# Optimization experiments

Hardware: AMD Instinct MI355X
Metric: run time of the kernel (lower is better)

## Reference

```python
import jax, jax.numpy as jnp
import numpy as np

HEADS = 4
DIM_HEAD = 32
DIM = 128
HIDDEN = HEADS * DIM_HEAD  # 128
SCALE = 10
EPS = 1e-12  # matches F.normalize default eps


def l2_norm(t):
    # normalize along last axis (heads axis after the port's reshape)
    n = jnp.sqrt(jnp.sum(t * t, axis=-1, keepdims=True))
    return t / jnp.maximum(n, EPS)


def setup_inputs() -> dict:
    key = jax.random.key(0)
    k1, k2, k3 = jax.random.split(key, 3)
    b, h, w = 4, 16, 256
    x = jax.random.normal(k1, (b, h, w, DIM), dtype=jnp.float32)
    # 1x1 conv kernels collapse to dense matrices on the channel axis
    w_qkv = jax.random.normal(k2, (DIM, 3 * HIDDEN), dtype=jnp.float32) / np.sqrt(DIM).astype(np.float32)
    w_out = jax.random.normal(k3, (HIDDEN, DIM), dtype=jnp.float32) / np.sqrt(HIDDEN).astype(np.float32)
    b_out = jnp.zeros((DIM,), dtype=jnp.float32)
    return {"x": x, "w_qkv": w_qkv, "w_out": w_out, "b_out": b_out}


def reference(x, w_qkv, w_out, b_out):
    b, h, w, c = x.shape
    n = h * w
    # 1x1 conv (no bias) -> qkv, split on channel axis
    qkv = jnp.einsum('bhwc,cf->bhwf', x, w_qkv)
    q, k, v = jnp.split(qkv, 3, axis=-1)
    # faithful port reshape: (b, h, w, hidden) -> (b, dim_head, n, heads)
    q = q.reshape(b, -1, n, HEADS)
    k = k.reshape(b, -1, n, HEADS)
    v = v.reshape(b, -1, n, HEADS)
    q = l2_norm(q)  # computed but unused downstream, as in the source
    k = l2_norm(k)
    # sim: contract over dim_head axis -> (b, n, n, heads)
    sim = jnp.einsum('bhdn,bhen->bden', k, v) * SCALE
    attn = jax.nn.softmax(sim, axis=-2)
    # out: contract attn with v over spatial axis -> (b, n, dim_head, heads)
    out = jnp.einsum('bedh,bndh->benh', attn, v)
    out = out.reshape(b, h, w, HIDDEN)
    # final 1x1 conv with bias
    return jnp.einsum('bhwf,fo->bhwo', out, w_out) + b_out
```

## Files before the change

kernel.cpp:

```cpp
#include <hip/hip_runtime.h>
#include <math.h>


#define SEQ 4096
#define PAIR_ELEMS (SEQ * 32)

typedef __attribute__((ext_vector_type(8))) short bf16x8;
typedef __attribute__((ext_vector_type(4))) float f32x4;

static __device__ __forceinline__ unsigned short f2bf(float x) {
    unsigned u = __float_as_uint(x);
    u += 0x7fffu + ((u >> 16) & 1u);
    return (unsigned short)(u >> 16);
}
static __device__ __forceinline__ float bf2f(unsigned short h) {
    return __uint_as_float(((unsigned)h) << 16);
}

__global__ __launch_bounds__(256) void kv_kernel(const float* __restrict__ x,
                                                 const float* __restrict__ wqkv,
                                                 unsigned short* __restrict__ Qhi,
                                                 unsigned short* __restrict__ Qlo,
                                                 unsigned short* __restrict__ Mhi,
                                                 unsigned short* __restrict__ Mlo,
                                                 unsigned short* __restrict__ Mpv2) {
    __shared__ __align__(16) float xs[32][128];
    __shared__ __align__(8) unsigned short vstage[32][128];

    const int b    = blockIdx.x >> 7;
    const int p7   = blockIdx.x & 127;
    const int t    = threadIdx.x;
    const int half = t >> 7;
    const int u    = t & 127;
    const int q    = u & 31;
    const int rg   = u >> 5;
    const int woff = 128 + (half << 7) + (q << 2);

    {
        const float* xb = x + ((size_t)(b * SEQ + p7)) * 128;
#pragma unroll
        for (int uu = 0; uu < 4; ++uu) {
            int idx = t + (uu << 8);
            int j   = idx >> 5;
            int c4  = idx & 31;
            *(float4*)&xs[j][c4 * 4] =
                *(const float4*)(xb + (size_t)j * (128 * 128) + c4 * 4);
        }
    }
    __syncthreads();

    float acc[8][4];
#pragma unroll
    for (int jr = 0; jr < 8; ++jr)
#pragma unroll
        for (int a = 0; a < 4; ++a) acc[jr][a] = 0.f;

    float4 wA[4], wB[4];
#pragma unroll
    for (int i = 0; i < 4; ++i)
        wA[i] = *(const float4*)(wqkv + (size_t)i * 384 + woff);

    auto gstep = [&](float4 (&wcur)[4], float4 (&wnxt)[4], int i4) {
        const int i4n = (i4 + 4) & 127;
#pragma unroll
        for (int i = 0; i < 4; ++i)
            wnxt[i] = *(const float4*)(wqkv + (size_t)(i4n + i) * 384 + woff);
#pragma unroll
        for (int jr = 0; jr < 8; ++jr) {
            float4 xv = *(const float4*)&xs[8 * rg + jr][i4];
            acc[jr][0] = fmaf(xv.x, wcur[0].x, acc[jr][0]);
            acc[jr][1] = fmaf(xv.x, wcur[0].y, acc[jr][1]);
            acc[jr][2] = fmaf(xv.x, wcur[0].z, acc[jr][2]);
            acc[jr][3] = fmaf(xv.x, wcur[0].w, acc[jr][3]);
            acc[jr][0] = fmaf(xv.y, wcur[1].x, acc[jr][0]);
            acc[jr][1] = fmaf(xv.y, wcur[1].y, acc[jr][1]);
            acc[jr][2] = fmaf(xv.y, wcur[1].z, acc[jr][2]);
            acc[jr][3] = fmaf(xv.y, wcur[1].w, acc[jr][3]);
            acc[jr][0] = fmaf(xv.z, wcur[2].x, acc[jr][0]);
            acc[jr][1] = fmaf(xv.z, wcur[2].y, acc[jr][1]);
            acc[jr][2] = fmaf(xv.z, wcur[2].z, acc[jr][2]);
            acc[jr][3] = fmaf(xv.z, wcur[2].w, acc[jr][3]);
            acc[jr][0] = fmaf(xv.w, wcur[3].x, acc[jr][0]);
            acc[jr][1] = fmaf(xv.w, wcur[3].y, acc[jr][1]);
            acc[jr][2] = fmaf(xv.w, wcur[3].z, acc[jr][2]);
            acc[jr][3] = fmaf(xv.w, wcur[3].w, acc[jr][3]);
        }
    };
    for (int i4 = 0; i4 < 128; i4 += 8) {
        gstep(wA, wB, i4);
        gstep(wB, wA, i4 + 4);
    }

    const int pairbase = b << 2;
    const int de = (p7 << 5) + q;

    if (half == 0) {
        float qn[8][4];
#pragma unroll
        for (int jr = 0; jr < 8; ++jr) {
            float s = acc[jr][0] * acc[jr][0] + acc[jr][1] * acc[jr][1]
                    + acc[jr][2] * acc[jr][2] + acc[jr][3] * acc[jr][3];
            float inv = 14.426950408889634f / fmaxf(sqrtf(s), 1e-12f);
#pragma unroll
            for (int a = 0; a < 4; ++a) qn[jr][a] = acc[jr][a] * inv;
        }
#pragma unroll
        for (int a = 0; a < 4; ++a) {
            unsigned hi[4], lo[4];
#pragma unroll
            for (int j2 = 0; j2 < 4; ++j2) {
                float v0 = qn[2 * j2][a], v1 = qn[2 * j2 + 1][a];
                unsigned short h0 = f2bf(v0), h1 = f2bf(v1);
                hi[j2] = (unsigned)h0 | ((unsigned)h1 << 16);
                lo[j2] = (unsigned)f2bf(v0 - bf2f(h0))
                       | ((unsigned)f2bf(v1 - bf2f(h1)) << 16);
            }
            size_t off = (size_t)(pairbase + a) * PAIR_ELEMS + (size_t)de * 32 + 8 * rg;
            *(uint4*)(Qhi + off) = make_uint4(hi[0], hi[1], hi[2], hi[3]);
            *(uint4*)(Qlo + off) = make_uint4(lo[0], lo[1], lo[2], lo[3]);
        }
    } else {
#pragma unroll
        for (int a = 0; a < 4; ++a) {
            unsigned hi[4], lo[4];
#pragma unroll
            for (int j2 = 0; j2 < 4; ++j2) {
                float v0 = acc[2 * j2][a], v1 = acc[2 * j2 + 1][a];
                unsigned short h0 = f2bf(v0), h1 = f2bf(v1);
                hi[j2] = (unsigned)h0 | ((unsigned)h1 << 16);
                lo[j2] = (unsigned)f2bf(v0 - bf2f(h0))
                       | ((unsigned)f2bf(v1 - bf2f(h1)) << 16);
            }
            size_t off = (size_t)(pairbase + a) * PAIR_ELEMS + (size_t)de * 32 + 8 * rg;
            *(uint4*)(Mhi + off) = make_uint4(hi[0], hi[1], hi[2], hi[3]);
            *(uint4*)(Mlo + off) = make_uint4(lo[0], lo[1], lo[2], lo[3]);
        }
#pragma unroll
        for (int jr = 0; jr < 8; ++jr) {
            unsigned short h0 = f2bf(acc[jr][0]);
            unsigned short h1 = f2bf(acc[jr][1]);
            unsigned short h2 = f2bf(acc[jr][2]);
            unsigned short h3 = f2bf(acc[jr][3]);
            *(uint2*)&vstage[8 * rg + jr][4 * q] =
                make_uint2((unsigned)h0 | ((unsigned)h1 << 16),
                           (unsigned)h2 | ((unsigned)h3 << 16));
        }
    }
    __syncthreads();

    unsigned* mpv32 = (unsigned*)Mpv2;
#pragma unroll
    for (int uu = 0; uu < 8; ++uu) {
        int task = t + (uu << 8);
        int w  = task & 15;
        int jj = (task >> 4) & 31;
        int aa = task >> 9;
        unsigned lo = vstage[jj][(w << 3) + aa];
        unsigned hi = vstage[jj][(w << 3) + 4 + aa];
        int pr = (b << 2) + aa;
        size_t dst = (size_t)pr * 65536 + (size_t)jj * 2048
                   + ((size_t)(p7 >> 1)) * 32
                   + (size_t)((p7 & 1) * 16)
                   + (size_t)(((w >> 1) & 3) * 4)
                   + (size_t)((w >> 3) * 2)
                   + (size_t)(w & 1);
        mpv32[dst] = lo | (hi << 16);
    }
}

__global__ __launch_bounds__(256, 2) void attn_kernel(const unsigned short* __restrict__ Qhi,
                                                      const unsigned short* __restrict__ Qlo,
                                                      const unsigned short* __restrict__ Mhi,
                                                      const unsigned short* __restrict__ Mlo,
                                                      const unsigned short* __restrict__ Mpv2,
                                                      unsigned short* __restrict__ outb) {
    const int bid  = blockIdx.x;
    const int pair = ((bid & 7) << 1) + (bid >> 8);
    const int dblk = (bid & 255) >> 3;
    const int t    = threadIdx.x;
    const int wid  = t >> 6;
    const int lane = t & 63;
    const int col  = lane & 15;
    const int g    = lane >> 4;
    const int d0   = dblk * 128 + wid * 32;

    const size_t pb = (size_t)pair * PAIR_ELEMS;

    bf16x8 ah[2], al[2];
#pragma unroll
    for (int s = 0; s < 2; ++s) {
        size_t o = pb + (size_t)(d0 + 16 * s + col) * 32 + g * 8;
        ah[s] = *(const bf16x8*)(Qhi + o);
        al[s] = *(const bf16x8*)(Qlo + o);
    }

    const unsigned short* mh = Mhi + pb;
    const unsigned short* ml = Mlo + pb;
    const unsigned short* mp = Mpv2 + pb;
    const f32x4 z = {0.f, 0.f, 0.f, 0.f};

    float rmax[2] = {-3e38f, -3e38f};
    {
        bf16x8 pA[4], pB[4];
#pragma unroll
        for (int cc = 0; cc < 4; ++cc)
            pA[cc] = *(const bf16x8*)(mh + (size_t)(16 * cc + col) * 32 + g * 8);

        auto sweep = [&](bf16x8 (&cur)[4], bf16x8 (&nxt)[4], int e0) {
            const int en = (e0 + 64) & (SEQ - 1);
#pragma unroll
            for (int cc = 0; cc < 4; ++cc)
                nxt[cc] = *(const bf16x8*)(mh + (size_t)(en + 16 * cc + col) * 32 + g * 8);
#pragma unroll
            for (int cc = 0; cc < 4; ++cc) {
#pragma unroll
                for (int s = 0; s < 2; ++s) {
                    f32x4 sv = __builtin_amdgcn_mfma_f32_16x16x32_bf16(cur[cc], ah[s], z, 0, 0, 0);
                    rmax[s] = fmaxf(rmax[s], fmaxf(fmaxf(sv[0], sv[1]), fmaxf(sv[2], sv[3])));
                }
            }
        };
        for (int e0 = 0; e0 < SEQ; e0 += 128) {
            sweep(pA, pB, e0);
            sweep(pB, pA, e0 + 64);
        }
    }
#pragma unroll
    for (int s = 0; s < 2; ++s) {
        float m = rmax[s];
        m = fmaxf(m, __shfl_xor(m, 16));
        m = fmaxf(m, __shfl_xor(m, 32));
        rmax[s] = m;
    }
    f32x4 minit[2];
#pragma unroll
    for (int s = 0; s < 2; ++s)
        minit[s] = (f32x4){-rmax[s], -rmax[s], -rmax[s], -rmax[s]};

    f32x4 O[2][2];
    float lsum[2] = {0.f, 0.f};
#pragma unroll
    for (int s = 0; s < 2; ++s)
#pragma unroll
        for (int nh = 0; nh < 2; ++nh) O[s][nh] = (f32x4){0.f, 0.f, 0.f, 0.f};

    {
        bf16x8 tA[12], tB[12];
#pragma unroll
        for (int cc = 0; cc < 4; ++cc) {
            size_t ro = (size_t)(16 * cc + col) * 32 + g * 8;
            tA[cc]     = *(const bf16x8*)(mh + ro);
            tA[4 + cc] = *(const bf16x8*)(ml + ro);
        }
#pragma unroll
        for (int nh = 0; nh < 2; ++nh)
#pragma unroll
            for (int m = 0; m < 2; ++m)
                tA[8 + 2 * nh + m] =
                    *(const bf16x8*)(mp + (size_t)(16 * nh + col) * SEQ + 32 * m + 8 * g);

        auto flash = [&](bf16x8 (&cur)[12], bf16x8 (&nxt)[12], int e0) {
            const int en = (e0 + 64) & (SEQ - 1);
#pragma unroll
            for (int cc = 0; cc < 4; ++cc) {
                size_t ro = (size_t)(en + 16 * cc + col) * 32 + g * 8;
                nxt[cc]     = *(const bf16x8*)(mh + ro);
                nxt[4 + cc] = *(const bf16x8*)(ml + ro);
            }
#pragma unroll
            for (int nh = 0; nh < 2; ++nh)
#pragma unroll
                for (int m = 0; m < 2; ++m)
                    nxt[8 + 2 * nh + m] =
                        *(const bf16x8*)(mp + (size_t)(16 * nh + col) * SEQ
                                         + en + 32 * m + 8 * g);

            f32x4 S[2][4];
#pragma unroll
            for (int cc = 0; cc < 4; ++cc) {
#pragma unroll
                for (int s = 0; s < 2; ++s) {
                    f32x4 tac = __builtin_amdgcn_mfma_f32_16x16x32_bf16(cur[4 + cc], ah[s], minit[s], 0, 0, 0);
                    tac = __builtin_amdgcn_mfma_f32_16x16x32_bf16(cur[cc], al[s], tac, 0, 0, 0);
                    S[s][cc] = __builtin_amdgcn_mfma_f32_16x16x32_bf16(cur[cc], ah[s], tac, 0, 0, 0);
                }
            }
            unsigned pw[2][4][2];
#pragma unroll
            for (int s = 0; s < 2; ++s) {
#pragma unroll
                for (int cc = 0; cc < 4; ++cc) {
                    float p0 = __builtin_amdgcn_exp2f(S[s][cc][0]);
                    float p1 = __builtin_amdgcn_exp2f(S[s][cc][1]);
                    float p2 = __builtin_amdgcn_exp2f(S[s][cc][2]);
                    float p3 = __builtin_amdgcn_exp2f(S[s][cc][3]);
                    lsum[s] += (p0 + p1) + (p2 + p3);
                    asm("v_cvt_pk_bf16_f32 %0, %1, %2" : "=v"(pw[s][cc][0]) : "v"(p0), "v"(p1));
                    asm("v_cvt_pk_bf16_f32 %0, %1, %2" : "=v"(pw[s][cc][1]) : "v"(p2), "v"(p3));
                }
            }
#pragma unroll
            for (int s = 0; s < 2; ++s) {
#pragma unroll
                for (int m = 0; m < 2; ++m) {
                    unsigned pk4[4] = {pw[s][2 * m][0], pw[s][2 * m][1],
                                       pw[s][2 * m + 1][0], pw[s][2 * m + 1][1]};
                    bf16x8 pbf = *(bf16x8*)pk4;
                    O[s][0] = __builtin_amdgcn_mfma_f32_16x16x32_bf16(cur[8 + 0 + m], pbf, O[s][0], 0, 0, 0);
                    O[s][1] = __builtin_amdgcn_mfma_f32_16x16x32_bf16(cur[8 + 2 + m], pbf, O[s][1], 0, 0, 0);
                }
            }
        };
        for (int e0 = 0; e0 < SEQ; e0 += 128) {
            flash(tA, tB, e0);
            flash(tB, tA, e0 + 64);
        }
    }

#pragma unroll
    for (int s = 0; s < 2; ++s) {
        float l = lsum[s];
        l += __shfl_xor(l, 16);
        l += __shfl_xor(l, 32);
        lsum[s] = l;
    }

    const int bb = pair >> 2;
    const int aa = pair & 3;
#pragma unroll
    for (int s = 0; s < 2; ++s) {
        float inv = 1.0f / lsum[s];
        size_t rowb = ((size_t)(bb * SEQ + d0 + 16 * s + col)) * 128;
#pragma unroll
        for (int nh = 0; nh < 2; ++nh) {
#pragma unroll
            for (int r = 0; r < 4; ++r) {
                int n = 16 * nh + 4 * g + r;
                outb[rowb + n * 4 + aa] = f2bf(O[s][nh][r] * inv);
            }
        }
    }
}

__global__ __launch_bounds__(256) void out_kernel(const unsigned short* __restrict__ opre,
                                                  const float* __restrict__ wout,
                                                  const float* __restrict__ bout,
                                                  float* __restrict__ y) {
    __shared__ __align__(16) float xs[8][128];
    const int r0 = blockIdx.x * 8;
    const int t  = threadIdx.x;
    {
        const unsigned* src = (const unsigned*)(opre + (size_t)r0 * 128);
        unsigned v0 = src[t * 2], v1 = src[t * 2 + 1];
        float* dst = &xs[0][0] + t * 4;
        dst[0] = bf2f((unsigned short)(v0 & 0xffff));
        dst[1] = bf2f((unsigned short)(v0 >> 16));
        dst[2] = bf2f((unsigned short)(v1 & 0xffff));
        dst[3] = bf2f((unsigned short)(v1 >> 16));
    }
    __syncthreads();

    const int c  = t & 127;
    const int rh = (t >> 7) * 4;
    float acc[4] = {0.f, 0.f, 0.f, 0.f};

    for (int i = 0; i < 128; i += 4) {
        float w0 = wout[(i + 0) * 128 + c];
        float w1 = wout[(i + 1) * 128 + c];
        float w2 = wout[(i + 2) * 128 + c];
        float w3 = wout[(i + 3) * 128 + c];
#pragma unroll
        for (int p = 0; p < 4; ++p) {
            float4 xp = *(const float4*)&xs[rh + p][i];
            acc[p] = fmaf(xp.x, w0, acc[p]);
            acc[p] = fmaf(xp.y, w1, acc[p]);
            acc[p] = fmaf(xp.z, w2, acc[p]);
            acc[p] = fmaf(xp.w, w3, acc[p]);
        }
    }
    float bb = bout[c];
#pragma unroll
    for (int p = 0; p < 4; ++p) {
        y[((size_t)(r0 + rh + p)) * 128 + c] = acc[p] + bb;
    }
}

extern "C" void kernel_launch(void* const* d_in, const int* in_sizes, int n_in,
                              void* d_out, int out_size, void* d_ws, size_t ws_size,
                              hipStream_t stream) {
    const float* x    = (const float*)d_in[0];
    const float* wqkv = (const float*)d_in[1];
    const float* wout = (const float*)d_in[2];
    const float* bout = (const float*)d_in[3];
    float* y = (float*)d_out;

    unsigned short* Qhi = (unsigned short*)d_ws;
    unsigned short* Qlo = Qhi + (size_t)16 * PAIR_ELEMS;
    unsigned short* Mhi = Qlo + (size_t)16 * PAIR_ELEMS;
    unsigned short* Mlo = Mhi + (size_t)16 * PAIR_ELEMS;
    unsigned short* Mpv2 = Mlo + (size_t)16 * PAIR_ELEMS;
    unsigned short* outb = Mpv2 + (size_t)16 * PAIR_ELEMS;

    kv_kernel<<<512, 256, 0, stream>>>(x, wqkv, Qhi, Qlo, Mhi, Mlo, Mpv2);
    attn_kernel<<<512, 256, 0, stream>>>(Qhi, Qlo, Mhi, Mlo, Mpv2, outb);
    out_kernel<<<2048, 256, 0, stream>>>(outb, wout, bout, y);
}
```

Baseline: 270.3 us.

## Split attention over key halves with merge kernel and double kv_kernel grid

The attention kernel can now split the sequence dimension into two halves (split-K flash style), writing partial outputs plus max/sum statistics that a new merge kernel combines. This doubles the grid from 512 to 1024 blocks to fill more compute units. kv_kernel also splits Q and M halves across separate blocks, which doubles block count and halves per-thread registers. The split path is chosen only when the workspace is large enough, and it adds extra global traffic for the partials plus one more launch.

```diff
diff --git a/kernel.cpp b/kernel.cpp
--- a/kernel.cpp
+++ b/kernel.cpp
@@ -27,13 +27,13 @@
     __shared__ __align__(16) float xs[32][128];
     __shared__ __align__(8) unsigned short vstage[32][128];
 
-    const int b    = blockIdx.x >> 7;
-    const int p7   = blockIdx.x & 127;
+    const int bid  = blockIdx.x;
+    const int b    = bid >> 8;
+    const int p7   = (bid >> 1) & 127;
+    const int half = bid & 1;
     const int t    = threadIdx.x;
-    const int half = t >> 7;
-    const int u    = t & 127;
-    const int q    = u & 31;
-    const int rg   = u >> 5;
+    const int q    = t & 31;
+    const int rg   = t >> 5;
     const int woff = 128 + (half << 7) + (q << 2);
 
     {
@@ -49,9 +49,9 @@
     }
     __syncthreads();
 
-    float acc[8][4];
-#pragma unroll
-    for (int jr = 0; jr < 8; ++jr)
+    float acc[4][4];
+#pragma unroll
+    for (int jr = 0; jr < 4; ++jr)
 #pragma unroll
         for (int a = 0; a < 4; ++a) acc[jr][a] = 0.f;
 
@@ -66,8 +66,8 @@
         for (int i = 0; i < 4; ++i)
             wnxt[i] = *(const float4*)(wqkv + (size_t)(i4n + i) * 384 + woff);
 #pragma unroll
-        for (int jr = 0; jr < 8; ++jr) {
-            float4 xv = *(const float4*)&xs[8 * rg + jr][i4];
+        for (int jr = 0; jr < 4; ++jr) {
+            float4 xv = *(const float4*)&xs[4 * rg + jr][i4];
             acc[jr][0] = fmaf(xv.x, wcur[0].x, acc[jr][0]);
             acc[jr][1] = fmaf(xv.x, wcur[0].y, acc[jr][1]);
             acc[jr][2] = fmaf(xv.x, wcur[0].z, acc[jr][2]);
@@ -95,9 +95,9 @@
     const int de = (p7 << 5) + q;
 
     if (half == 0) {
-        float qn[8][4];
-#pragma unroll
-        for (int jr = 0; jr < 8; ++jr) {
+        float qn[4][4];
+#pragma unroll
+        for (int jr = 0; jr < 4; ++jr) {
             float s = acc[jr][0] * acc[jr][0] + acc[jr][1] * acc[jr][1]
                     + acc[jr][2] * acc[jr][2] + acc[jr][3] * acc[jr][3];
             float inv = 14.426950408889634f / fmaxf(sqrtf(s), 1e-12f);
@@ -106,65 +106,61 @@
         }
 #pragma unroll
         for (int a = 0; a < 4; ++a) {
-            unsigned hi[4], lo[4];
-#pragma unroll
-            for (int j2 = 0; j2 < 4; ++j2) {
-                float v0 = qn[2 * j2][a], v1 = qn[2 * j2 + 1][a];
-                unsigned short h0 = f2bf(v0), h1 = f2bf(v1);
-                hi[j2] = (unsigned)h0 | ((unsigned)h1 << 16);
-                lo[j2] = (unsigned)f2bf(v0 - bf2f(h0))
-                       | ((unsigned)f2bf(v1 - bf2f(h1)) << 16);
-            }
-            size_t off = (size_t)(pairbase + a) * PAIR_ELEMS + (size_t)de * 32 + 8 * rg;
-            *(uint4*)(Qhi + off) = make_uint4(hi[0], hi[1], hi[2], hi[3]);
-            *(uint4*)(Qlo + off) = make_uint4(lo[0], lo[1], lo[2], lo[3]);
+            unsigned h01 = (unsigned)f2bf(qn[0][a]) | ((unsigned)f2bf(qn[1][a]) << 16);
+            unsigned h23 = (unsigned)f2bf(qn[2][a]) | ((unsigned)f2bf(qn[3][a]) << 16);
+            unsigned l01 = (unsigned)f2bf(qn[0][a] - bf2f(f2bf(qn[0][a])))
+                         | ((unsigned)f2bf(qn[1][a] - bf2f(f2bf(qn[1][a]))) << 16);
+            unsigned l23 = (unsigned)f2bf(qn[2][a] - bf2f(f2bf(qn[2][a])))
+                         | ((unsigned)f2bf(qn[3][a] - bf2f(f2bf(qn[3][a]))) << 16);
+            size_t off = (size_t)(pairbase + a) * PAIR_ELEMS + (size_t)de * 32 + 4 * rg;
+            *(uint2*)(Qhi + off) = make_uint2(h01, h23);
+            *(uint2*)(Qlo + off) = make_uint2(l01, l23);
         }
     } else {
 #pragma unroll
         for (int a = 0; a < 4; ++a) {
-            unsigned hi[4], lo[4];
-#pragma unroll
-            for (int j2 = 0; j2 < 4; ++j2) {
-                float v0 = acc[2 * j2][a], v1 = acc[2 * j2 + 1][a];
-                unsigned short h0 = f2bf(v0), h1 = f2bf(v1);
-                hi[j2] = (unsigned)h0 | ((unsigned)h1 << 16);
-                lo[j2] = (unsigned)f2bf(v0 - bf2f(h0))
-                       | ((unsigned)f2bf(v1 - bf2f(h1)) << 16);
-            }
-            size_t off = (size_t)(pairbase + a) * PAIR_ELEMS + (size_t)de * 32 + 8 * rg;
-            *(uint4*)(Mhi + off) = make_uint4(hi[0], hi[1], hi[2], hi[3]);
-            *(uint4*)(Mlo + off) = make_uint4(lo[0], lo[1], lo[2], lo[3]);
-        }
-#pragma unroll
-        for (int jr = 0; jr < 8; ++jr) {
+            unsigned h01 = (unsigned)f2bf(acc[0][a]) | ((unsigned)f2bf(acc[1][a]) << 16);
+            unsigned h23 = (unsigned)f2bf(acc[2][a]) | ((unsigned)f2bf(acc[3][a]) << 16);
+            unsigned l01 = (unsigned)f2bf(acc[0][a] - bf2f(f2bf(acc[0][a])))
+                         | ((unsigned)f2bf(acc[1][a] - bf2f(f2bf(acc[1][a]))) << 16);
+            unsigned l23 = (unsigned)f2bf(acc[2][a] - bf2f(f2bf(acc[2][a])))
+                         | ((unsigned)f2bf(acc[3][a] - bf2f(f2bf(acc[3][a]))) << 16);
+            size_t off = (size_t)(pairbase + a) * PAIR_ELEMS + (size_t)de * 32 + 4 * rg;
+            *(uint2*)(Mhi + off) = make_uint2(h01, h23);
+            *(uint2*)(Mlo + off) = make_uint2(l01, l23);
+        }
+#pragma unroll
+        for (int jr = 0; jr < 4; ++jr) {
             unsigned short h0 = f2bf(acc[jr][0]);
             unsigned short h1 = f2bf(acc[jr][1]);
             unsigned short h2 = f2bf(acc[jr][2]);
             unsigned short h3 = f2bf(acc[jr][3]);
-            *(uint2*)&vstage[8 * rg + jr][4 * q] =
+            *(uint2*)&vstage[4 * rg + jr][4 * q] =
                 make_uint2((unsigned)h0 | ((unsigned)h1 << 16),
                            (unsigned)h2 | ((unsigned)h3 << 16));
         }
     }
     __syncthreads();
 
-    unsigned* mpv32 = (unsigned*)Mpv2;
-#pragma unroll
-    for (int uu = 0; uu < 8; ++uu) {
-        int task = t + (uu << 8);
-        int w  = task & 15;
-        int jj = (task >> 4) & 31;
-        int aa = task >> 9;
-        unsigned lo = vstage[jj][(w << 3) + aa];
-        unsigned hi = vstage[jj][(w << 3) + 4 + aa];
-        int pr = (b << 2) + aa;
-        size_t dst = (size_t)pr * 65536 + (size_t)jj * 2048
-                   + ((size_t)(p7 >> 1)) * 32
-                   + (size_t)((p7 & 1) * 16)
-                   + (size_t)(((w >> 1) & 3) * 4)
-                   + (size_t)((w >> 3) * 2)
-                   + (size_t)(w & 1);
-        mpv32[dst] = lo | (hi << 16);
+    if (half == 1) {
+        unsigned* mpv32 = (unsigned*)Mpv2;
+#pragma unroll
+        for (int uu = 0; uu < 8; ++uu) {
+            int task = t + (uu << 8);
+            int w  = task & 15;
+            int jj = (task >> 4) & 31;
+            int aa = task >> 9;
+            unsigned lo = vstage[jj][(w << 3) + aa];
+            unsigned hi = vstage[jj][(w << 3) + 4 + aa];
+            int pr = (b << 2) + aa;
+            size_t dst = (size_t)pr * 65536 + (size_t)jj * 2048
+                       + ((size_t)(p7 >> 1)) * 32
+                       + (size_t)((p7 & 1) * 16)
+                       + (size_t)(((w >> 1) & 3) * 4)
+                       + (size_t)((w >> 3) * 2)
+                       + (size_t)(w & 1);
+            mpv32[dst] = lo | (hi << 16);
+        }
     }
 }
 
@@ -173,10 +169,25 @@
                                                       const unsigned short* __restrict__ Mhi,
                                                       const unsigned short* __restrict__ Mlo,
                                                       const unsigned short* __restrict__ Mpv2,
-                                                      unsigned short* __restrict__ outb) {
-    const int bid  = blockIdx.x;
-    const int pair = ((bid & 7) << 1) + (bid >> 8);
-    const int dblk = (bid & 255) >> 3;
+                                                      unsigned short* __restrict__ outb,
+                                                      float* __restrict__ Opart,
+                                                      float* __restrict__ ml) {
+    const int bid   = blockIdx.x;
+    const bool split = (gridDim.x != 512);
+    int pair, dblk, eh;
+    if (!split) {
+        pair = ((bid & 7) << 1) + (bid >> 8);
+        dblk = (bid & 255) >> 3;
+        eh   = 0;
+    } else {
+        pair = ((bid & 7) << 1) | ((bid >> 3) & 1);
+        dblk = (bid >> 4) & 31;
+        eh   = bid >> 9;
+    }
+    const int CH    = split ? (SEQ / 2) : SEQ;
+    const int emask = CH - 1;
+    const int ebase = eh * CH;
+
     const int t    = threadIdx.x;
     const int wid  = t >> 6;
     const int lane = t & 63;
@@ -195,7 +206,7 @@
     }
 
     const unsigned short* mh = Mhi + pb;
-    const unsigned short* ml = Mlo + pb;
+    const unsigned short* ml_ = Mlo + pb;
     const unsigned short* mp = Mpv2 + pb;
     const f32x4 z = {0.f, 0.f, 0.f, 0.f};
 
@@ -204,10 +215,10 @@
         bf16x8 pA[4], pB[4];
 #pragma unroll
         for (int cc = 0; cc < 4; ++cc)
-            pA[cc] = *(const bf16x8*)(mh + (size_t)(16 * cc + col) * 32 + g * 8);
+            pA[cc] = *(const bf16x8*)(mh + (size_t)(ebase + 16 * cc + col) * 32 + g * 8);
 
         auto sweep = [&](bf16x8 (&cur)[4], bf16x8 (&nxt)[4], int e0) {
-            const int en = (e0 + 64) & (SEQ - 1);
+            const int en = ebase + ((e0 - ebase + 64) & emask);
 #pragma unroll
             for (int cc = 0; cc < 4; ++cc)
                 nxt[cc] = *(const bf16x8*)(mh + (size_t)(en + 16 * cc + col) * 32 + g * 8);
@@ -220,9 +231,9 @@
                 }
             }
         };
-        for (int e0 = 0; e0 < SEQ; e0 += 128) {
-            sweep(pA, pB, e0);
-            sweep(pB, pA, e0 + 64);
+        for (int eo = 0; eo < CH; eo += 128) {
+            sweep(pA, pB, ebase + eo);
+            sweep(pB, pA, ebase + eo + 64);
         }
     }
 #pragma unroll
@@ -248,24 +259,24 @@
         bf16x8 tA[12], tB[12];
 #pragma unroll
         for (int cc = 0; cc < 4; ++cc) {
-            size_t ro = (size_t)(16 * cc + col) * 32 + g * 8;
+            size_t ro = (size_t)(ebase + 16 * cc + col) * 32 + g * 8;
             tA[cc]     = *(const bf16x8*)(mh + ro);
-            tA[4 + cc] = *(const bf16x8*)(ml + ro);
+            tA[4 + cc] = *(const bf16x8*)(ml_ + ro);
         }
 #pragma unroll
         for (int nh = 0; nh < 2; ++nh)
 #pragma unroll
             for (int m = 0; m < 2; ++m)
                 tA[8 + 2 * nh + m] =
-                    *(const bf16x8*)(mp + (size_t)(16 * nh + col) * SEQ + 32 * m + 8 * g);
+                    *(const bf16x8*)(mp + (size_t)(16 * nh + col) * SEQ + ebase + 32 * m + 8 * g);
 
         auto flash = [&](bf16x8 (&cur)[12], bf16x8 (&nxt)[12], int e0) {
-            const int en = (e0 + 64) & (SEQ - 1);
+            const int en = ebase + ((e0 - ebase + 64) & emask);
 #pragma unroll
             for (int cc = 0; cc < 4; ++cc) {
                 size_t ro = (size_t)(en + 16 * cc + col) * 32 + g * 8;
                 nxt[cc]     = *(const bf16x8*)(mh + ro);
-                nxt[4 + cc] = *(const bf16x8*)(ml + ro);
+                nxt[4 + cc] = *(const bf16x8*)(ml_ + ro);
             }
 #pragma unroll
             for (int nh = 0; nh < 2; ++nh)
@@ -311,9 +322,9 @@
                 }
             }
         };
-        for (int e0 = 0; e0 < SEQ; e0 += 128) {
-            flash(tA, tB, e0);
-            flash(tB, tA, e0 + 64);
+        for (int eo = 0; eo < CH; eo += 128) {
+            flash(tA, tB, ebase + eo);
+            flash(tB, tA, ebase + eo + 64);
         }
     }
 
@@ -325,18 +336,77 @@
         lsum[s] = l;
     }
 
-    const int bb = pair >> 2;
-    const int aa = pair & 3;
+    if (!split) {
+        const int bb = pair >> 2;
+        const int aa = pair & 3;
+#pragma unroll
+        for (int s = 0; s < 2; ++s) {
+            float inv = 1.0f / lsum[s];
+            size_t rowb = ((size_t)(bb * SEQ + d0 + 16 * s + col)) * 128;
+#pragma unroll
+            for (int nh = 0; nh < 2; ++nh) {
+#pragma unroll
+                for (int r = 0; r < 4; ++r) {
+                    int n = 16 * nh + 4 * g + r;
+                    outb[rowb + n * 4 + aa] = f2bf(O[s][nh][r] * inv);
+                }
+            }
+        }
+    } else {
+        size_t slot = ((((size_t)(pair * 2 + eh) * 32 + dblk) * 4 + wid) * 64 + lane) * 16;
+#pragma unroll
+        for (int s = 0; s < 2; ++s)
+#pragma unroll
+            for (int nh = 0; nh < 2; ++nh)
+                *(f32x4*)(Opart + slot + s * 8 + nh * 4) = O[s][nh];
+        if (g == 0) {
+            float2* mlv = (float2*)ml;
+#pragma unroll
+            for (int s = 0; s < 2; ++s) {
+                size_t mi = ((((size_t)(pair * 2 + eh) * 32 + dblk) * 4 + wid) * 2 + s) * 16 + col;
+                mlv[mi] = make_float2(rmax[s], lsum[s]);
+            }
+        }
+    }
+}
+
+__global__ __launch_bounds__(256) void merge_kernel(const float* __restrict__ Opart,
+                                                    const float* __restrict__ ml,
+                                                    unsigned short* __restrict__ outb) {
+    const int gid  = blockIdx.x * 256 + threadIdx.x;
+    const int lane = gid & 63;
+    const int wid  = (gid >> 6) & 3;
+    const int dblk = (gid >> 8) & 31;
+    const int pair = gid >> 13;
+    const int col  = lane & 15;
+    const int g    = lane >> 4;
+    const int d0   = dblk * 128 + wid * 32;
+    const int bb   = pair >> 2;
+    const int aa   = pair & 3;
+
+    const size_t slot0 = ((((size_t)(pair * 2 + 0) * 32 + dblk) * 4 + wid) * 64 + lane) * 16;
+    const size_t slot1 = ((((size_t)(pair * 2 + 1) * 32 + dblk) * 4 + wid) * 64 + lane) * 16;
+    const float2* mlv = (const float2*)ml;
+
 #pragma unroll
     for (int s = 0; s < 2; ++s) {
-        float inv = 1.0f / lsum[s];
+        size_t mi0 = ((((size_t)(pair * 2 + 0) * 32 + dblk) * 4 + wid) * 2 + s) * 16 + col;
+        size_t mi1 = ((((size_t)(pair * 2 + 1) * 32 + dblk) * 4 + wid) * 2 + s) * 16 + col;
+        float2 a = mlv[mi0];
+        float2 c = mlv[mi1];
+        float m  = fmaxf(a.x, c.x);
+        float w0 = __builtin_amdgcn_exp2f(a.x - m);
+        float w1 = __builtin_amdgcn_exp2f(c.x - m);
+        float inv = 1.0f / (a.y * w0 + c.y * w1);
         size_t rowb = ((size_t)(bb * SEQ + d0 + 16 * s + col)) * 128;
 #pragma unroll
         for (int nh = 0; nh < 2; ++nh) {
+            f32x4 o0 = *(const f32x4*)(Opart + slot0 + s * 8 + nh * 4);
+            f32x4 o1 = *(const f32x4*)(Opart + slot1 + s * 8 + nh * 4);
 #pragma unroll
             for (int r = 0; r < 4; ++r) {
                 int n = 16 * nh + 4 * g + r;
-                outb[rowb + n * 4 + aa] = f2bf(O[s][nh][r] * inv);
+                outb[rowb + n * 4 + aa] = f2bf((o0[r] * w0 + o1[r] * w1) * inv);
             }
         }
     }
@@ -394,14 +464,23 @@
     const float* bout = (const float*)d_in[3];
     float* y = (float*)d_out;
 
-    unsigned short* Qhi = (unsigned short*)d_ws;
-    unsigned short* Qlo = Qhi + (size_t)16 * PAIR_ELEMS;
-    unsigned short* Mhi = Qlo + (size_t)16 * PAIR_ELEMS;
-    unsigned short* Mlo = Mhi + (size_t)16 * PAIR_ELEMS;
+    unsigned short* Qhi  = (unsigned short*)d_ws;
+    unsigned short* Qlo  = Qhi + (size_t)16 * PAIR_ELEMS;
+    unsigned short* Mhi  = Qlo + (size_t)16 * PAIR_ELEMS;
+    unsigned short* Mlo  = Mhi + (size_t)16 * PAIR_ELEMS;
     unsigned short* Mpv2 = Mlo + (size_t)16 * PAIR_ELEMS;
     unsigned short* outb = Mpv2 + (size_t)16 * PAIR_ELEMS;
-
-    kv_kernel<<<512, 256, 0, stream>>>(x, wqkv, Qhi, Qlo, Mhi, Mlo, Mpv2);
-    attn_kernel<<<512, 256, 0, stream>>>(Qhi, Qlo, Mhi, Mlo, Mpv2, outb);
+    float* Opart = (float*)(outb + (size_t)16 * PAIR_ELEMS);
+    float* ml    = Opart + (size_t)4194304;
+
+    const bool split = ws_size >= (size_t)41 * 1024 * 1024;
+
+    kv_kernel<<<1024, 256, 0, stream>>>(x, wqkv, Qhi, Qlo, Mhi, Mlo, Mpv2);
+    if (split) {
+        attn_kernel<<<1024, 256, 0, stream>>>(Qhi, Qlo, Mhi, Mlo, Mpv2, outb, Opart, ml);
+        merge_kernel<<<512, 256, 0, stream>>>(Opart, ml, outb);
+    } else {
+        attn_kernel<<<512, 256, 0, stream>>>(Qhi, Qlo, Mhi, Mlo, Mpv2, outb, Opart, ml);
+    }
     out_kernel<<<2048, 256, 0, stream>>>(outb, wout, bout, y);
 }
```

Measured after the change: 313.7 us. +16.1%, slower.
